# Kernel optimization log

Hardware: AMD Instinct MI355X
Metric: run time of the kernel (lower is better)

Reference implementation:

```python
import jax, jax.numpy as jnp
import numpy as np

LATENT = 1024
HID = 512
J = 24
# SMPL kinematic tree (parent[0] = -1 is the root, unused in the loop)
PARENT = [-1, 0, 0, 0, 1, 2, 3, 4, 5, 6, 7, 8, 9, 9, 9, 12, 13, 14, 16, 17, 18, 19, 20, 21]
EPS = 1e-12  # F.normalize default eps


def setup_inputs() -> dict:
    key = jax.random.key(0)
    k1, k2, k3, k4, k5 = jax.random.split(key, 5)
    B = 32768
    # Kaiming-uniform-ish init scales for the Linear layers
    s1 = 1.0 / np.sqrt(LATENT)
    s2 = 1.0 / np.sqrt(HID)
    return {
        "z": jax.random.normal(k1, (B, LATENT), dtype=jnp.float32),
        "W1": jax.random.uniform(k2, (LATENT, HID), minval=-s1, maxval=s1, dtype=jnp.float32),
        "b1": jax.random.uniform(k3, (HID,), minval=-s1, maxval=s1, dtype=jnp.float32),
        "W2": jax.random.uniform(k4, (HID, (J - 1) * 4), minval=-s2, maxval=s2, dtype=jnp.float32),
        "b2": jax.random.uniform(k5, ((J - 1) * 4,), minval=-s2, maxval=s2, dtype=jnp.float32),
    }


def reference(z, W1, b1, W2, b2):
    B = z.shape[0]
    h = jax.nn.silu(z @ W1 + b1)                    # [B, 512]
    raw = (h @ W2 + b2).reshape(B, J - 1, 4)        # [B, J-1, 4]
    vec = raw[..., :3]                              # [B, J-1, 3]
    norm = jnp.linalg.norm(vec, axis=-1, keepdims=True)
    direction = vec / jnp.maximum(norm, EPS)        # F.normalize(dim=-1)
    length = jax.nn.softplus(raw[..., 3])           # [B, J-1]
    child_off = direction * length[..., None]       # [B, J-1, 3]
    offsets = jnp.concatenate(
        [jnp.zeros((B, 1, 3), dtype=z.dtype), child_off], axis=1
    )                                                # [B, J, 3]
    # Static-tree forward kinematics: unroll the (small, fixed) joint loop.
    joints_list = [jnp.zeros((B, 3), dtype=z.dtype)]
    for j in range(1, J):
        joints_list.append(joints_list[PARENT[j]] + offsets[:, j])
    joints = jnp.stack(joints_list, axis=1)          # [B, J, 3]
    return (joints, offsets, length)
```

## Files before the change

### kernel.cpp

```cpp
#include <hip/hip_runtime.h>
#include <hip/hip_bf16.h>
#include <stdint.h>

#define BROWS 32768
#define LATENT 1024
#define HID 512

typedef float f32x4 __attribute__((ext_vector_type(4)));
typedef __bf16 bf16x8 __attribute__((ext_vector_type(8)));
typedef unsigned short us8 __attribute__((ext_vector_type(8)));

__device__ __forceinline__ void gload16(const void* g, void* l) {
  __builtin_amdgcn_global_load_lds(
      (__attribute__((address_space(1))) void*)g,
      (__attribute__((address_space(3))) void*)l, 16, 0, 0);
}

__device__ __forceinline__ void split_bf16(float x, unsigned short& hi, unsigned short& lo) {
  __bf16 h = (__bf16)x;
  float r = x - (float)h;
  __bf16 l = (__bf16)r;
  hi = __builtin_bit_cast(unsigned short, h);
  lo = __builtin_bit_cast(unsigned short, l);
}

__device__ __forceinline__ f32x4 mfma16(bf16x8 a, bf16x8 b, f32x4 c) {
  return __builtin_amdgcn_mfma_f32_16x16x32_bf16(a, b, c, 0, 0, 0);
}

__device__ __forceinline__ bf16x8 ldfrag(const unsigned short* p) {
  return __builtin_bit_cast(bf16x8, *(const us8*)p);
}

__global__ __launch_bounds__(256) void k_prep_w1t(const float* __restrict__ W1,
                                                  unsigned short* __restrict__ hi,
                                                  unsigned short* __restrict__ lo) {
  __shared__ float t[64][65];
  const int i = threadIdx.x;
  const int k0 = blockIdx.x * 64;
  const int n0 = blockIdx.y * 64;
#pragma unroll
  for (int s = 0; s < 4; s++) {
    const int r = s * 16 + (i >> 4);
    const int c = (i & 15) * 4;
    float4 v = *(const float4*)&W1[(size_t)(k0 + r) * HID + n0 + c];
    t[r][c] = v.x; t[r][c + 1] = v.y; t[r][c + 2] = v.z; t[r][c + 3] = v.w;
  }
  __syncthreads();
#pragma unroll
  for (int s = 0; s < 4; s++) {
    const int n = s * 16 + (i >> 4);
    const int k = (i & 15) * 4;
    unsigned short h[4], l[4];
#pragma unroll
    for (int j = 0; j < 4; j++) split_bf16(t[k + j][n], h[j], l[j]);
    *(ushort4*)&hi[(size_t)(n0 + n) * LATENT + k0 + k] = make_ushort4(h[0], h[1], h[2], h[3]);
    *(ushort4*)&lo[(size_t)(n0 + n) * LATENT + k0 + k] = make_ushort4(l[0], l[1], l[2], l[3]);
  }
}

__global__ __launch_bounds__(256) void k_prep_w2t(const float* __restrict__ W2,
                                                  unsigned short* __restrict__ hi,
                                                  unsigned short* __restrict__ lo) {
  const int idx = blockIdx.x * 256 + threadIdx.x;
  const int n = idx >> 9, k = idx & 511;
  const float v = (n < 92) ? W2[(size_t)k * 92 + n] : 0.0f;
  unsigned short h, l;
  split_bf16(v, h, l);
  hi[idx] = h;
  lo[idx] = l;
}

__global__ __launch_bounds__(256, 2) void k_gemm1(
    const float* __restrict__ z, const unsigned short* __restrict__ w1h,
    const unsigned short* __restrict__ w1l, const float* __restrict__ b1,
    unsigned short* __restrict__ hh, unsigned short* __restrict__ hl) {
  __shared__ unsigned short Ah[2][4096], Al[2][4096];
  __shared__ unsigned short Bh[2][4096], Bl[2][4096];

  const int tid = threadIdx.x;
  const int bid = blockIdx.x;
  const int swz = (bid & 7) * 128 + (bid >> 3);
  const int m0 = (swz >> 2) * 128;
  const int n0 = (swz & 3) * 128;

  const int w = tid >> 6, lane = tid & 63;
  const int wr = w >> 1, wc = w & 1;
  const int l15 = lane & 15, lg = lane >> 4;

  const int arow = tid >> 3;
  const int acol = (tid & 7) << 2;
  const int brow = tid >> 2;
  const int bc8 = (tid & 3) << 3;

  const float* zb = z + (size_t)(m0 + arow) * LATENT + acol;
  const unsigned short* w1hb = w1h + (size_t)(n0 + brow) * LATENT + bc8;
  const unsigned short* w1lb = w1l + (size_t)(n0 + brow) * LATENT + bc8;

  f32x4 acc[4][4] = {};
  float4 zr[4];

#define G1_STAGE_Z(kt) { \
    const float* p_ = zb + (kt) * 32; \
    zr[0] = *(const float4*)(p_); \
    zr[1] = *(const float4*)(p_ + 32 * LATENT); \
    zr[2] = *(const float4*)(p_ + 64 * LATENT); \
    zr[3] = *(const float4*)(p_ + 96 * LATENT); }

#define G1_STAGE_B(kt, bf) { \
    gload16(w1hb + (kt) * 32,               &Bh[bf][(w << 9)]); \
    gload16(w1hb + (kt) * 32 + 64 * LATENT, &Bh[bf][2048 + (w << 9)]); \
    gload16(w1lb + (kt) * 32,               &Bl[bf][(w << 9)]); \
    gload16(w1lb + (kt) * 32 + 64 * LATENT, &Bl[bf][2048 + (w << 9)]); }

#define G1_WRITE_A(bf) { \
    _Pragma("unroll") \
    for (int s_ = 0; s_ < 4; s_++) { \
      unsigned short h0, h1, h2, h3, l0, l1, l2, l3; \
      split_bf16(zr[s_].x, h0, l0); split_bf16(zr[s_].y, h1, l1); \
      split_bf16(zr[s_].z, h2, l2); split_bf16(zr[s_].w, h3, l3); \
      const int o_ = ((s_ * 32 + arow) << 5) + acol; \
      *(ushort4*)&Ah[bf][o_] = make_ushort4(h0, h1, h2, h3); \
      *(ushort4*)&Al[bf][o_] = make_ushort4(l0, l1, l2, l3); \
    } }

#define G1_COMPUTE(bf) { \
    bf16x8 ah[4], al[4], bh[4], bl[4]; \
    _Pragma("unroll") \
    for (int mf = 0; mf < 4; mf++) { \
      const int o_ = ((wr * 64 + mf * 16 + l15) << 5) + (lg << 3); \
      ah[mf] = ldfrag(&Ah[bf][o_]); \
      al[mf] = ldfrag(&Al[bf][o_]); \
    } \
    _Pragma("unroll") \
    for (int nf = 0; nf < 4; nf++) { \
      const int o_ = ((wc * 64 + nf * 16 + l15) << 5) + (lg << 3); \
      bh[nf] = ldfrag(&Bh[bf][o_]); \
      bl[nf] = ldfrag(&Bl[bf][o_]); \
    } \
    _Pragma("unroll") \
    for (int mf = 0; mf < 4; mf++) { \
      _Pragma("unroll") \
      for (int nf = 0; nf < 4; nf++) { \
        acc[mf][nf] = mfma16(ah[mf], bh[nf], acc[mf][nf]); \
        acc[mf][nf] = mfma16(al[mf], bh[nf], acc[mf][nf]); \
        acc[mf][nf] = mfma16(ah[mf], bl[nf], acc[mf][nf]); \
      } } }

  G1_STAGE_Z(0);
  G1_STAGE_B(0, 0);
  G1_WRITE_A(0);
  __syncthreads();

#pragma unroll 2
  for (int kt = 0; kt < 32; kt++) {
    const int cur = kt & 1, nx = cur ^ 1;
    if (kt < 31) {
      G1_STAGE_Z(kt + 1);
      G1_STAGE_B(kt + 1, nx);
    }
    G1_COMPUTE(cur);
    if (kt < 31) G1_WRITE_A(nx);
    __syncthreads();
  }

  float b1v[4];
#pragma unroll
  for (int nf = 0; nf < 4; nf++) b1v[nf] = b1[n0 + wc * 64 + nf * 16 + l15];

#pragma unroll
  for (int mf = 0; mf < 4; mf++) {
#pragma unroll
    for (int nf = 0; nf < 4; nf++) {
#pragma unroll
      for (int r = 0; r < 4; r++) {
        const int gm = m0 + wr * 64 + mf * 16 + (lg << 2) + r;
        const int gn = n0 + wc * 64 + nf * 16 + l15;
        const float x = acc[mf][nf][r] + b1v[nf];
        const float hval = x / (1.0f + expf(-x));
        unsigned short hi_, lo_;
        split_bf16(hval, hi_, lo_);
        const size_t o = (size_t)gm * HID + gn;
        hh[o] = hi_;
        hl[o] = lo_;
      }
    }
  }
}

__global__ __launch_bounds__(256, 2) void k_gemm2(
    const unsigned short* __restrict__ hh, const unsigned short* __restrict__ hl,
    const unsigned short* __restrict__ w2h, const unsigned short* __restrict__ w2l,
    const float* __restrict__ b2, float* __restrict__ out) {
  __shared__ unsigned short Ah[2][2048], Al[2][2048];
  __shared__ unsigned short Bh[2][4096], Bl[2][4096];
  __shared__ float raw[64][97];

  const int tid = threadIdx.x;
  const int m0 = blockIdx.x * 64;
  const int w = tid >> 6, lane = tid & 63;
  const int wr = w >> 1, wc = w & 1;
  const int l15 = lane & 15, lg = lane >> 4;
  const int arow = tid >> 2, ac8 = (tid & 3) << 3;

  const unsigned short* hhb = hh + (size_t)(m0 + arow) * HID + ac8;
  const unsigned short* hlb = hl + (size_t)(m0 + arow) * HID + ac8;
  const unsigned short* w2hb = w2h + (size_t)arow * HID + ac8;
  const unsigned short* w2lb = w2l + (size_t)arow * HID + ac8;

  f32x4 acc[2][3] = {};

#define G2_STAGE(kt, bf) { \
    gload16(hhb + (kt) * 32, &Ah[bf][(w << 9)]); \
    gload16(hlb + (kt) * 32, &Al[bf][(w << 9)]); \
    gload16(w2hb + (kt) * 32,            &Bh[bf][(w << 9)]); \
    gload16(w2hb + (kt) * 32 + 64 * HID, &Bh[bf][2048 + (w << 9)]); \
    gload16(w2lb + (kt) * 32,            &Bl[bf][(w << 9)]); \
    gload16(w2lb + (kt) * 32 + 64 * HID, &Bl[bf][2048 + (w << 9)]); }

#define G2_COMPUTE(bf) { \
    bf16x8 ah[2], al[2], bh[3], bl[3]; \
    _Pragma("unroll") \
    for (int mf = 0; mf < 2; mf++) { \
      const int o_ = ((wr * 32 + mf * 16 + l15) << 5) + (lg << 3); \
      ah[mf] = ldfrag(&Ah[bf][o_]); \
      al[mf] = ldfrag(&Al[bf][o_]); \
    } \
    _Pragma("unroll") \
    for (int nf = 0; nf < 3; nf++) { \
      const int o_ = ((wc * 48 + nf * 16 + l15) << 5) + (lg << 3); \
      bh[nf] = ldfrag(&Bh[bf][o_]); \
      bl[nf] = ldfrag(&Bl[bf][o_]); \
    } \
    _Pragma("unroll") \
    for (int mf = 0; mf < 2; mf++) { \
      _Pragma("unroll") \
      for (int nf = 0; nf < 3; nf++) { \
        acc[mf][nf] = mfma16(ah[mf], bh[nf], acc[mf][nf]); \
        acc[mf][nf] = mfma16(al[mf], bh[nf], acc[mf][nf]); \
        acc[mf][nf] = mfma16(ah[mf], bl[nf], acc[mf][nf]); \
      } } }

  G2_STAGE(0, 0);
  __syncthreads();
#pragma unroll 2
  for (int kt = 0; kt < 16; kt++) {
    const int cur = kt & 1, nx = cur ^ 1;
    if (kt < 15) G2_STAGE(kt + 1, nx);
    G2_COMPUTE(cur);
    __syncthreads();
  }

#pragma unroll
  for (int mf = 0; mf < 2; mf++) {
#pragma unroll
    for (int nf = 0; nf < 3; nf++) {
#pragma unroll
      for (int r = 0; r < 4; r++) {
        const int ml = wr * 32 + mf * 16 + (lg << 2) + r;
        const int nl = wc * 48 + nf * 16 + l15;
        raw[ml][nl] = acc[mf][nf][r];
      }
    }
  }
  __syncthreads();

  const size_t OFFB = (size_t)BROWS * 72;
  const size_t LENB = (size_t)BROWS * 144;

  for (int task = tid; task < 64 * 24; task += 256) {
    const int row = task / 24;
    const int j = task - row * 24;
    const int gm = m0 + row;
    float* orow = out + OFFB + (size_t)gm * 72;
    if (j == 0) {
      orow[0] = 0.0f; orow[1] = 0.0f; orow[2] = 0.0f;
    } else {
      const int c0 = (j - 1) * 4;
      const float vx = raw[row][c0 + 0] + b2[c0 + 0];
      const float vy = raw[row][c0 + 1] + b2[c0 + 1];
      const float vz = raw[row][c0 + 2] + b2[c0 + 2];
      const float wv = raw[row][c0 + 3] + b2[c0 + 3];
      const float nrm = sqrtf(vx * vx + vy * vy + vz * vz);
      const float inv = 1.0f / fmaxf(nrm, 1e-12f);
      const float len = fmaxf(wv, 0.0f) + log1pf(expf(-fabsf(wv)));
      const float sc = inv * len;
      const float ox = vx * sc, oy = vy * sc, oz = vz * sc;
      orow[j * 3 + 0] = ox; orow[j * 3 + 1] = oy; orow[j * 3 + 2] = oz;
      out[LENB + (size_t)gm * 23 + (j - 1)] = len;
      raw[row][c0 + 0] = ox; raw[row][c0 + 1] = oy; raw[row][c0 + 2] = oz;
    }
  }
  __syncthreads();

  if (tid < 64) {
    constexpr int PAR[24] = {-1, 0, 0, 0, 1, 2, 3, 4, 5, 6, 7, 8,
                             9, 9, 9, 12, 13, 14, 16, 17, 18, 19, 20, 21};
    const int gm = m0 + tid;
    float e[72];
    e[0] = 0.0f; e[1] = 0.0f; e[2] = 0.0f;
#pragma unroll
    for (int j = 1; j < 24; j++) {
      const int p = PAR[j];
      const int c0 = (j - 1) * 4;
      e[3 * j + 0] = e[3 * p + 0] + raw[tid][c0 + 0];
      e[3 * j + 1] = e[3 * p + 1] + raw[tid][c0 + 1];
      e[3 * j + 2] = e[3 * p + 2] + raw[tid][c0 + 2];
    }
    float4* jo = (float4*)(out + (size_t)gm * 72);
#pragma unroll
    for (int q = 0; q < 18; q++)
      jo[q] = make_float4(e[4 * q + 0], e[4 * q + 1], e[4 * q + 2], e[4 * q + 3]);
  }
}

extern "C" void kernel_launch(void* const* d_in, const int* in_sizes, int n_in,
                              void* d_out, int out_size, void* d_ws, size_t ws_size,
                              hipStream_t stream) {
  const float* z = (const float*)d_in[0];
  const float* W1 = (const float*)d_in[1];
  const float* b1 = (const float*)d_in[2];
  const float* W2 = (const float*)d_in[3];
  const float* b2 = (const float*)d_in[4];
  float* out = (float*)d_out;

  char* ws = (char*)d_ws;
  unsigned short* w1h = (unsigned short*)(ws);
  unsigned short* w1l = (unsigned short*)(ws + (1 << 20));
  unsigned short* w2h = (unsigned short*)(ws + (2 << 20));
  unsigned short* w2l = (unsigned short*)(ws + (2 << 20) + 131072);
  unsigned short* hh = (unsigned short*)(ws + ((size_t)4 << 20));
  unsigned short* hl = (unsigned short*)(ws + ((size_t)4 << 20) + ((size_t)32 << 20));

  hipLaunchKernelGGL(k_prep_w1t, dim3(16, 8), dim3(256), 0, stream, W1, w1h, w1l);
  hipLaunchKernelGGL(k_prep_w2t, dim3(256), dim3(256), 0, stream, W2, w2h, w2l);
  hipLaunchKernelGGL(k_gemm1, dim3(1024), dim3(256), 0, stream, z, w1h, w1l, b1, hh, hl);
  hipLaunchKernelGGL(k_gemm2, dim3(512), dim3(256), 0, stream, hh, hl, w2h, w2l, b2, out);
}
```

Measured before the change: 164.6 us.

## Restructure gemm1 pipeline with swizzled LDS, 8x2 wave tiling and fine-grained waitcnt scheduling

Rewrites the first GEMM kernel's main loop. All operands now live in one byte-addressed LDS buffer with XOR-swizzled layouts to avoid bank conflicts. Each wave covers 128 rows by 32 columns instead of a 2x2 wave grid of 64x64 tiles. Each K step is split into three MFMA phases (hi*hi, lo*hi, hi*lo), with global loads for the next tile interleaved between them and explicit vmcnt/lgkmcnt waits, sched_barriers and s_setprio. The block swizzle changes so blocks sharing an N tile run together. The aim is better overlap of global memory traffic with MFMA work and fewer LDS conflicts, at the risk of fragile manual wait counts and more A-fragment register pressure.

Measured after the change: 166.7 us. About the same (+1.3%).

```diff
diff --git a/kernel.cpp b/kernel.cpp
--- a/kernel.cpp
+++ b/kernel.cpp
@@ -28,7 +28,7 @@
   return __builtin_amdgcn_mfma_f32_16x16x32_bf16(a, b, c, 0, 0, 0);
 }
 
-__device__ __forceinline__ bf16x8 ldfrag(const unsigned short* p) {
+__device__ __forceinline__ bf16x8 ldfrag(const void* p) {
   return __builtin_bit_cast(bf16x8, *(const us8*)p);
 }
 
@@ -75,107 +75,153 @@
     const float* __restrict__ z, const unsigned short* __restrict__ w1h,
     const unsigned short* __restrict__ w1l, const float* __restrict__ b1,
     unsigned short* __restrict__ hh, unsigned short* __restrict__ hl) {
-  __shared__ unsigned short Ah[2][4096], Al[2][4096];
-  __shared__ unsigned short Bh[2][4096], Bl[2][4096];
+  __shared__ __attribute__((aligned(16))) unsigned short lds_u[32768];
+  char* lb = (char*)lds_u;
 
   const int tid = threadIdx.x;
   const int bid = blockIdx.x;
   const int swz = (bid & 7) * 128 + (bid >> 3);
-  const int m0 = (swz >> 2) * 128;
-  const int n0 = (swz & 3) * 128;
-
-  const int w = tid >> 6, lane = tid & 63;
-  const int wr = w >> 1, wc = w & 1;
-  const int l15 = lane & 15, lg = lane >> 4;
-
-  const int arow = tid >> 3;
-  const int acol = (tid & 7) << 2;
-  const int brow = tid >> 2;
-  const int bc8 = (tid & 3) << 3;
-
-  const float* zb = z + (size_t)(m0 + arow) * LATENT + acol;
-  const unsigned short* w1hb = w1h + (size_t)(n0 + brow) * LATENT + bc8;
-  const unsigned short* w1lb = w1l + (size_t)(n0 + brow) * LATENT + bc8;
-
-  f32x4 acc[4][4] = {};
+  const int nb = swz >> 8;
+  const int mb = swz & 255;
+  const int m0 = mb * 128;
+  const int n0g = nb * 128;
+
+  const int wv = tid >> 6, l = tid & 63;
+  const int l15 = l & 15, lg = l >> 4;
+
+  const int abase = l15 * 64 + ((lg ^ ((l15 >> 1) & 3)) << 4);
+
+  const float* zbase = z + (size_t)(m0 + (tid >> 3)) * LATENT + (tid & 7) * 4;
+  const int wbyte = (tid >> 3) * 64 + (((tid & 7) * 8) ^ (((tid >> 4) & 3) << 4));
+
+  const size_t bsrc = (size_t)(n0g + 32 * wv + (l >> 2)) * LATENT +
+                      ((((l & 3) ^ ((l >> 3) & 3))) << 3);
+
+  f32x4 acc[8][2] = {};
   float4 zr[4];
-
-#define G1_STAGE_Z(kt) { \
-    const float* p_ = zb + (kt) * 32; \
-    zr[0] = *(const float4*)(p_); \
-    zr[1] = *(const float4*)(p_ + 32 * LATENT); \
-    zr[2] = *(const float4*)(p_ + 64 * LATENT); \
-    zr[3] = *(const float4*)(p_ + 96 * LATENT); }
-
-#define G1_STAGE_B(kt, bf) { \
-    gload16(w1hb + (kt) * 32,               &Bh[bf][(w << 9)]); \
-    gload16(w1hb + (kt) * 32 + 64 * LATENT, &Bh[bf][2048 + (w << 9)]); \
-    gload16(w1lb + (kt) * 32,               &Bl[bf][(w << 9)]); \
-    gload16(w1lb + (kt) * 32 + 64 * LATENT, &Bl[bf][2048 + (w << 9)]); }
-
-#define G1_WRITE_A(bf) { \
-    _Pragma("unroll") \
-    for (int s_ = 0; s_ < 4; s_++) { \
-      unsigned short h0, h1, h2, h3, l0, l1, l2, l3; \
-      split_bf16(zr[s_].x, h0, l0); split_bf16(zr[s_].y, h1, l1); \
-      split_bf16(zr[s_].z, h2, l2); split_bf16(zr[s_].w, h3, l3); \
-      const int o_ = ((s_ * 32 + arow) << 5) + acol; \
-      *(ushort4*)&Ah[bf][o_] = make_ushort4(h0, h1, h2, h3); \
-      *(ushort4*)&Al[bf][o_] = make_ushort4(l0, l1, l2, l3); \
-    } }
-
-#define G1_COMPUTE(bf) { \
-    bf16x8 ah[4], al[4], bh[4], bl[4]; \
-    _Pragma("unroll") \
-    for (int mf = 0; mf < 4; mf++) { \
-      const int o_ = ((wr * 64 + mf * 16 + l15) << 5) + (lg << 3); \
-      ah[mf] = ldfrag(&Ah[bf][o_]); \
-      al[mf] = ldfrag(&Al[bf][o_]); \
-    } \
-    _Pragma("unroll") \
-    for (int nf = 0; nf < 4; nf++) { \
-      const int o_ = ((wc * 64 + nf * 16 + l15) << 5) + (lg << 3); \
-      bh[nf] = ldfrag(&Bh[bf][o_]); \
-      bl[nf] = ldfrag(&Bl[bf][o_]); \
-    } \
-    _Pragma("unroll") \
-    for (int mf = 0; mf < 4; mf++) { \
-      _Pragma("unroll") \
-      for (int nf = 0; nf < 4; nf++) { \
-        acc[mf][nf] = mfma16(ah[mf], bh[nf], acc[mf][nf]); \
-        acc[mf][nf] = mfma16(al[mf], bh[nf], acc[mf][nf]); \
-        acc[mf][nf] = mfma16(ah[mf], bl[nf], acc[mf][nf]); \
-      } } }
-
-  G1_STAGE_Z(0);
-  G1_STAGE_B(0, 0);
-  G1_WRITE_A(0);
-  __syncthreads();
+  bf16x8 ah[8], bhf[2], blf[2];
+
+#define AHO 0
+#define ALO 8192
+#define BHO 16384
+#define BLO 24576
+
+#define ISSUE_A(kt1)                                                         \
+  {                                                                          \
+    _Pragma("unroll") for (int i_ = 0; i_ < 4; i_++)                         \
+        zr[i_] = *(const float4*)(zbase + (size_t)(32 * i_) * LATENT + (kt1) * 32); \
+  }
+
+#define ISSUE_B(arr, kt1, dstoff, j_)                                        \
+  gload16(arr + bsrc + (size_t)(16 * (j_)) * LATENT + (kt1) * 32,            \
+          lb + (dstoff) + (wv * 2 + (j_)) * 1024);
+
+#define WRITE_A(dstAh, dstAl)                                                \
+  {                                                                          \
+    _Pragma("unroll") for (int i_ = 0; i_ < 4; i_++) {                       \
+      unsigned short h0, h1, h2, h3, q0, q1, q2, q3;                         \
+      split_bf16(zr[i_].x, h0, q0); split_bf16(zr[i_].y, h1, q1);            \
+      split_bf16(zr[i_].z, h2, q2); split_bf16(zr[i_].w, h3, q3);            \
+      *(ushort4*)(lb + (dstAh) + wbyte + i_ * 2048) = make_ushort4(h0, h1, h2, h3); \
+      *(ushort4*)(lb + (dstAl) + wbyte + i_ * 2048) = make_ushort4(q0, q1, q2, q3); \
+    }                                                                        \
+  }
+
+#define LD_AFRAGS(dst, roff)                                                 \
+  {                                                                          \
+    _Pragma("unroll") for (int mf = 0; mf < 8; mf++)                         \
+        dst[mf] = ldfrag(lb + (roff) + abase + mf * 1024);                   \
+  }
+
+#define LD_BFRAGS(dst, roff)                                                 \
+  {                                                                          \
+    _Pragma("unroll") for (int nf = 0; nf < 2; nf++)                         \
+        dst[nf] = ldfrag(lb + (roff) + wv * 2048 + nf * 1024 + abase);       \
+  }
+
+#define DO_MFMA(AF, BF)                                                      \
+  {                                                                          \
+    __builtin_amdgcn_s_setprio(1);                                           \
+    _Pragma("unroll") for (int mf = 0; mf < 8; mf++)                         \
+        _Pragma("unroll") for (int nf = 0; nf < 2; nf++)                     \
+            acc[mf][nf] = mfma16(AF[mf], BF[nf], acc[mf][nf]);               \
+    __builtin_amdgcn_s_setprio(0);                                           \
+  }
+
+#define SBAR  __builtin_amdgcn_s_barrier()
+#define SCH0  __builtin_amdgcn_sched_barrier(0)
+
+  ISSUE_A(0);
+  SCH0;
+  ISSUE_B(w1h, 0, BHO, 0); ISSUE_B(w1h, 0, BHO, 1);
+  ISSUE_B(w1l, 0, BLO, 0); ISSUE_B(w1l, 0, BLO, 1);
+  SCH0;
+  asm volatile("s_waitcnt vmcnt(4)" ::: "memory");
+  SCH0;
+  WRITE_A(AHO, ALO);
+  asm volatile("s_waitcnt lgkmcnt(0)" ::: "memory");
+  SBAR; SCH0;
 
 #pragma unroll 2
-  for (int kt = 0; kt < 32; kt++) {
-    const int cur = kt & 1, nx = cur ^ 1;
-    if (kt < 31) {
-      G1_STAGE_Z(kt + 1);
-      G1_STAGE_B(kt + 1, nx);
-    }
-    G1_COMPUTE(cur);
-    if (kt < 31) G1_WRITE_A(nx);
-    __syncthreads();
-  }
-
-  float b1v[4];
-#pragma unroll
-  for (int nf = 0; nf < 4; nf++) b1v[nf] = b1[n0 + wc * 64 + nf * 16 + l15];
-
-#pragma unroll
-  for (int mf = 0; mf < 4; mf++) {
-#pragma unroll
-    for (int nf = 0; nf < 4; nf++) {
+  for (int t = 0; t < 32; ++t) {
+    const int cur = (t & 1) * 32768;
+    const int nxt = cur ^ 32768;
+    const bool last = (t == 31);
+
+    asm volatile("s_waitcnt vmcnt(1)" ::: "memory");
+    SCH0;
+    LD_AFRAGS(ah, cur + AHO);
+    LD_BFRAGS(bhf, cur + BHO);
+    if (!last) {
+      ISSUE_A(t + 1);
+      SCH0;
+      ISSUE_B(w1h, t + 1, nxt + BHO, 0);
+    }
+    SBAR; SCH0;
+    DO_MFMA(ah, bhf);
+    SBAR; SCH0;
+
+    {
+      bf16x8 alf[8];
+      LD_AFRAGS(alf, cur + ALO);
+      if (!last) {
+        ISSUE_B(w1h, t + 1, nxt + BHO, 1);
+        ISSUE_B(w1l, t + 1, nxt + BLO, 0);
+      }
+      SBAR; SCH0;
+      DO_MFMA(alf, bhf);
+      SBAR; SCH0;
+    }
+
+    if (!last) { asm volatile("s_waitcnt vmcnt(7)" ::: "memory"); }
+    else       { asm volatile("s_waitcnt vmcnt(0)" ::: "memory"); }
+    SCH0;
+    LD_BFRAGS(blf, cur + BLO);
+    if (!last) {
+      ISSUE_B(w1l, t + 1, nxt + BLO, 1);
+      asm volatile("s_waitcnt vmcnt(3)" ::: "memory");
+      SCH0;
+      WRITE_A(nxt + AHO, nxt + ALO);
+      asm volatile("s_waitcnt lgkmcnt(0)" ::: "memory");
+      SCH0;
+    }
+    SBAR; SCH0;
+    DO_MFMA(ah, blf);
+    SBAR; SCH0;
+  }
+
+  float b1v[2];
+#pragma unroll
+  for (int nf = 0; nf < 2; nf++) b1v[nf] = b1[n0g + wv * 32 + nf * 16 + l15];
+
+#pragma unroll
+  for (int mf = 0; mf < 8; mf++)
+#pragma unroll
+    for (int nf = 0; nf < 2; nf++)
 #pragma unroll
       for (int r = 0; r < 4; r++) {
-        const int gm = m0 + wr * 64 + mf * 16 + (lg << 2) + r;
-        const int gn = n0 + wc * 64 + nf * 16 + l15;
+        const int gm = m0 + mf * 16 + (lg << 2) + r;
+        const int gn = n0g + wv * 32 + nf * 16 + l15;
         const float x = acc[mf][nf][r] + b1v[nf];
         const float hval = x / (1.0f + expf(-x));
         unsigned short hi_, lo_;
@@ -184,8 +230,11 @@
         hh[o] = hi_;
         hl[o] = lo_;
       }
-    }
-  }
+
+#undef AHO
+#undef ALO
+#undef BHO
+#undef BLO
 }
 
 __global__ __launch_bounds__(256, 2) void k_gemm2(
```

## Restructure gemm1 into 256x256 tiles with swizzled fused hi/lo LDS layout

Applied to the files above, without the earlier changes.

The GEMM1 tile grows from 128x128 with 4 waves to 256x256 with 8 waves in 128KB of dynamic LDS. W1 is pre-packed into a fused, XOR-swizzled hi/lo bf16 layout so that B loads go straight to LDS and fragment reads avoid bank conflicts. The main loop is rescheduled with explicit waitcnt, raw barriers, setprio around the MFMA clusters, and prefetch of z two steps ahead, to raise data reuse and overlap loads with compute. In exchange, register pressure rises (32 accumulators per wave), and with only 256 blocks occupancy is low, which risks tail imbalance across the 256 CUs.

Result: faster. 151.1 us (-8.2%).

```diff
diff --git a/kernel.cpp b/kernel.cpp
--- a/kernel.cpp
+++ b/kernel.cpp
@@ -28,35 +28,28 @@
   return __builtin_amdgcn_mfma_f32_16x16x32_bf16(a, b, c, 0, 0, 0);
 }
 
-__device__ __forceinline__ bf16x8 ldfrag(const unsigned short* p) {
+__device__ __forceinline__ bf16x8 ldfrag(const void* p) {
   return __builtin_bit_cast(bf16x8, *(const us8*)p);
 }
 
-__global__ __launch_bounds__(256) void k_prep_w1t(const float* __restrict__ W1,
-                                                  unsigned short* __restrict__ hi,
-                                                  unsigned short* __restrict__ lo) {
-  __shared__ float t[64][65];
-  const int i = threadIdx.x;
-  const int k0 = blockIdx.x * 64;
-  const int n0 = blockIdx.y * 64;
-#pragma unroll
-  for (int s = 0; s < 4; s++) {
-    const int r = s * 16 + (i >> 4);
-    const int c = (i & 15) * 4;
-    float4 v = *(const float4*)&W1[(size_t)(k0 + r) * HID + n0 + c];
-    t[r][c] = v.x; t[r][c + 1] = v.y; t[r][c + 2] = v.z; t[r][c + 3] = v.w;
-  }
-  __syncthreads();
-#pragma unroll
-  for (int s = 0; s < 4; s++) {
-    const int n = s * 16 + (i >> 4);
-    const int k = (i & 15) * 4;
-    unsigned short h[4], l[4];
-#pragma unroll
-    for (int j = 0; j < 4; j++) split_bf16(t[k + j][n], h[j], l[j]);
-    *(ushort4*)&hi[(size_t)(n0 + n) * LATENT + k0 + k] = make_ushort4(h[0], h[1], h[2], h[3]);
-    *(ushort4*)&lo[(size_t)(n0 + n) * LATENT + k0 + k] = make_ushort4(l[0], l[1], l[2], l[3]);
-  }
+__global__ __launch_bounds__(256) void k_prep_w1f(const float* __restrict__ W1,
+                                                  unsigned short* __restrict__ w1f) {
+  const int n = blockIdx.x;
+  const int t = threadIdx.x;
+  const int kt = t >> 3, ls = t & 7;
+  const int p = ls ^ (n & 7);
+  const int k0 = kt * 32 + (ls & 3) * 8;
+  unsigned short v[8];
+#pragma unroll
+  for (int e = 0; e < 8; e++) {
+    const float x = W1[(size_t)(k0 + e) * HID + n];
+    unsigned short h, q;
+    split_bf16(x, h, q);
+    v[e] = (ls < 4) ? h : q;
+  }
+  unsigned short* dst = w1f + ((size_t)n * 32 + kt) * 64 + p * 8;
+  *(ushort4*)(dst) = make_ushort4(v[0], v[1], v[2], v[3]);
+  *(ushort4*)(dst + 4) = make_ushort4(v[4], v[5], v[6], v[7]);
 }
 
 __global__ __launch_bounds__(256) void k_prep_w2t(const float* __restrict__ W2,
@@ -71,111 +64,137 @@
   lo[idx] = l;
 }
 
-__global__ __launch_bounds__(256, 2) void k_gemm1(
-    const float* __restrict__ z, const unsigned short* __restrict__ w1h,
-    const unsigned short* __restrict__ w1l, const float* __restrict__ b1,
+__global__ __launch_bounds__(512, 2) void k_gemm1(
+    const float* __restrict__ z, const unsigned short* __restrict__ w1f,
+    const float* __restrict__ b1,
     unsigned short* __restrict__ hh, unsigned short* __restrict__ hl) {
-  __shared__ unsigned short Ah[2][4096], Al[2][4096];
-  __shared__ unsigned short Bh[2][4096], Bl[2][4096];
+  extern __shared__ __align__(16) char lb[];
 
   const int tid = threadIdx.x;
   const int bid = blockIdx.x;
-  const int swz = (bid & 7) * 128 + (bid >> 3);
-  const int m0 = (swz >> 2) * 128;
-  const int n0 = (swz & 3) * 128;
-
-  const int w = tid >> 6, lane = tid & 63;
-  const int wr = w >> 1, wc = w & 1;
-  const int l15 = lane & 15, lg = lane >> 4;
+  const int swzb = (bid & 7) * 32 + (bid >> 3);
+  const int mb = swzb >> 1, nbk = swzb & 1;
+  const int m0 = mb * 256, n0g = nbk * 256;
+
+  const int wv = tid >> 6, l = tid & 63;
+  const int wr = wv >> 2, wc = wv & 3;
+  const int l15 = l & 15, lg = l >> 4;
+  const int xr = l15 & 7;
+
+  const int ahB = (wr * 128 + l15) * 128 + ((lg ^ xr) << 4);
+  const int alB = (wr * 128 + l15) * 128 + ((((4 | lg) ^ xr)) << 4);
+  const int bhB = 32768 + (wc * 64 + l15) * 128 + ((lg ^ xr) << 4);
+  const int blB = 32768 + (wc * 64 + l15) * 128 + ((((4 | lg) ^ xr)) << 4);
 
   const int arow = tid >> 3;
-  const int acol = (tid & 7) << 2;
-  const int brow = tid >> 2;
-  const int bc8 = (tid & 3) << 3;
-
-  const float* zb = z + (size_t)(m0 + arow) * LATENT + acol;
-  const unsigned short* w1hb = w1h + (size_t)(n0 + brow) * LATENT + bc8;
-  const unsigned short* w1lb = w1l + (size_t)(n0 + brow) * LATENT + bc8;
-
-  f32x4 acc[4][4] = {};
+  const int kc4 = tid & 7;
+  const int xw = arow & 7;
+  const int hi_off = (((kc4 >> 1) ^ xw) << 4) + (kc4 & 1) * 8;
+  const int lo_off = ((((4 | (kc4 >> 1)) ^ xw)) << 4) + (kc4 & 1) * 8;
+  const float* zb = z + (size_t)(m0 + arow) * LATENT + kc4 * 4;
+
+  const unsigned short* bsrc =
+      w1f + ((size_t)(n0g + wv * 32 + (l >> 3)) * 32) * 64 + (l & 7) * 8;
+
+  f32x4 acc[8][4] = {};
   float4 zr[4];
 
-#define G1_STAGE_Z(kt) { \
-    const float* p_ = zb + (kt) * 32; \
-    zr[0] = *(const float4*)(p_); \
-    zr[1] = *(const float4*)(p_ + 32 * LATENT); \
-    zr[2] = *(const float4*)(p_ + 64 * LATENT); \
-    zr[3] = *(const float4*)(p_ + 96 * LATENT); }
-
-#define G1_STAGE_B(kt, bf) { \
-    gload16(w1hb + (kt) * 32,               &Bh[bf][(w << 9)]); \
-    gload16(w1hb + (kt) * 32 + 64 * LATENT, &Bh[bf][2048 + (w << 9)]); \
-    gload16(w1lb + (kt) * 32,               &Bl[bf][(w << 9)]); \
-    gload16(w1lb + (kt) * 32 + 64 * LATENT, &Bl[bf][2048 + (w << 9)]); }
-
-#define G1_WRITE_A(bf) { \
-    _Pragma("unroll") \
-    for (int s_ = 0; s_ < 4; s_++) { \
-      unsigned short h0, h1, h2, h3, l0, l1, l2, l3; \
-      split_bf16(zr[s_].x, h0, l0); split_bf16(zr[s_].y, h1, l1); \
-      split_bf16(zr[s_].z, h2, l2); split_bf16(zr[s_].w, h3, l3); \
-      const int o_ = ((s_ * 32 + arow) << 5) + acol; \
-      *(ushort4*)&Ah[bf][o_] = make_ushort4(h0, h1, h2, h3); \
-      *(ushort4*)&Al[bf][o_] = make_ushort4(l0, l1, l2, l3); \
-    } }
-
-#define G1_COMPUTE(bf) { \
-    bf16x8 ah[4], al[4], bh[4], bl[4]; \
-    _Pragma("unroll") \
-    for (int mf = 0; mf < 4; mf++) { \
-      const int o_ = ((wr * 64 + mf * 16 + l15) << 5) + (lg << 3); \
-      ah[mf] = ldfrag(&Ah[bf][o_]); \
-      al[mf] = ldfrag(&Al[bf][o_]); \
-    } \
-    _Pragma("unroll") \
-    for (int nf = 0; nf < 4; nf++) { \
-      const int o_ = ((wc * 64 + nf * 16 + l15) << 5) + (lg << 3); \
-      bh[nf] = ldfrag(&Bh[bf][o_]); \
-      bl[nf] = ldfrag(&Bl[bf][o_]); \
-    } \
-    _Pragma("unroll") \
-    for (int mf = 0; mf < 4; mf++) { \
-      _Pragma("unroll") \
-      for (int nf = 0; nf < 4; nf++) { \
-        acc[mf][nf] = mfma16(ah[mf], bh[nf], acc[mf][nf]); \
-        acc[mf][nf] = mfma16(al[mf], bh[nf], acc[mf][nf]); \
-        acc[mf][nf] = mfma16(ah[mf], bl[nf], acc[mf][nf]); \
-      } } }
-
-  G1_STAGE_Z(0);
-  G1_STAGE_B(0, 0);
-  G1_WRITE_A(0);
-  __syncthreads();
+#define LOAD_ZR(kt1)                                                          \
+  {                                                                           \
+    _Pragma("unroll") for (int i_ = 0; i_ < 4; i_++)                          \
+        zr[i_] = *(const float4*)(zb + (size_t)(64 * i_) * LATENT + (kt1) * 32); \
+  }
+
+#define WRITE_A(bufo)                                                         \
+  {                                                                           \
+    _Pragma("unroll") for (int i_ = 0; i_ < 4; i_++) {                        \
+      unsigned short h0, h1, h2, h3, q0, q1, q2, q3;                          \
+      split_bf16(zr[i_].x, h0, q0); split_bf16(zr[i_].y, h1, q1);             \
+      split_bf16(zr[i_].z, h2, q2); split_bf16(zr[i_].w, h3, q3);             \
+      char* rp = lb + (bufo) + (arow + 64 * i_) * 128;                        \
+      *(ushort4*)(rp + hi_off) = make_ushort4(h0, h1, h2, h3);                \
+      *(ushort4*)(rp + lo_off) = make_ushort4(q0, q1, q2, q3);                \
+    }                                                                         \
+  }
+
+#define GLOAD_B(bufo, kt1)                                                    \
+  {                                                                           \
+    _Pragma("unroll") for (int j_ = 0; j_ < 4; j_++)                          \
+        gload16(bsrc + (size_t)j_ * 16384 + (kt1) * 64,                       \
+                lb + (bufo) + 32768 + (wv * 32 + j_ * 8) * 128);              \
+  }
+
+#define MCLUSTER(AF, BF)                                                      \
+  {                                                                           \
+    __builtin_amdgcn_s_setprio(1);                                            \
+    _Pragma("unroll") for (int mf = 0; mf < 8; mf++)                          \
+        _Pragma("unroll") for (int nf = 0; nf < 4; nf++)                      \
+            acc[mf][nf] = mfma16(AF[mf], BF[nf], acc[mf][nf]);                \
+    __builtin_amdgcn_s_setprio(0);                                            \
+  }
+
+  GLOAD_B(0, 0);
+  LOAD_ZR(0);
+  asm volatile("s_waitcnt vmcnt(0)" ::: "memory");
+  WRITE_A(0);
+  LOAD_ZR(1);
+  asm volatile("s_waitcnt lgkmcnt(0)" ::: "memory");
+  __builtin_amdgcn_s_barrier();
+  __builtin_amdgcn_sched_barrier(0);
 
 #pragma unroll 2
-  for (int kt = 0; kt < 32; kt++) {
-    const int cur = kt & 1, nx = cur ^ 1;
-    if (kt < 31) {
-      G1_STAGE_Z(kt + 1);
-      G1_STAGE_B(kt + 1, nx);
-    }
-    G1_COMPUTE(cur);
-    if (kt < 31) G1_WRITE_A(nx);
-    __syncthreads();
+  for (int t = 0; t < 32; ++t) {
+    const int cb = (t & 1) * 65536;
+    const int nb2 = cb ^ 65536;
+
+    bf16x8 ah[8], bh[4];
+#pragma unroll
+    for (int mf = 0; mf < 8; mf++) ah[mf] = ldfrag(lb + cb + ahB + mf * 2048);
+#pragma unroll
+    for (int nf = 0; nf < 4; nf++) bh[nf] = ldfrag(lb + cb + bhB + nf * 2048);
+
+    if (t < 31) {
+      WRITE_A(nb2);
+      GLOAD_B(nb2, t + 1);
+      asm volatile("" ::: "memory");
+      if (t < 30) LOAD_ZR(t + 2);
+    }
+
+    MCLUSTER(ah, bh);
+
+    {
+      bf16x8 alf[8];
+#pragma unroll
+      for (int mf = 0; mf < 8; mf++) alf[mf] = ldfrag(lb + cb + alB + mf * 2048);
+      MCLUSTER(alf, bh);
+    }
+
+    {
+      bf16x8 blf[4];
+#pragma unroll
+      for (int nf = 0; nf < 4; nf++) blf[nf] = ldfrag(lb + cb + blB + nf * 2048);
+      MCLUSTER(ah, blf);
+    }
+
+    if (t < 30) { asm volatile("s_waitcnt vmcnt(4)" ::: "memory"); }
+    else        { asm volatile("s_waitcnt vmcnt(0)" ::: "memory"); }
+    asm volatile("s_waitcnt lgkmcnt(0)" ::: "memory");
+    __builtin_amdgcn_s_barrier();
+    __builtin_amdgcn_sched_barrier(0);
   }
 
   float b1v[4];
 #pragma unroll
-  for (int nf = 0; nf < 4; nf++) b1v[nf] = b1[n0 + wc * 64 + nf * 16 + l15];
-
-#pragma unroll
-  for (int mf = 0; mf < 4; mf++) {
-#pragma unroll
-    for (int nf = 0; nf < 4; nf++) {
+  for (int nf = 0; nf < 4; nf++) b1v[nf] = b1[n0g + wc * 64 + nf * 16 + l15];
+
+#pragma unroll
+  for (int mf = 0; mf < 8; mf++)
+#pragma unroll
+    for (int nf = 0; nf < 4; nf++)
 #pragma unroll
       for (int r = 0; r < 4; r++) {
-        const int gm = m0 + wr * 64 + mf * 16 + (lg << 2) + r;
-        const int gn = n0 + wc * 64 + nf * 16 + l15;
+        const int gm = m0 + wr * 128 + mf * 16 + (lg << 2) + r;
+        const int gn = n0g + wc * 64 + nf * 16 + l15;
         const float x = acc[mf][nf][r] + b1v[nf];
         const float hval = x / (1.0f + expf(-x));
         unsigned short hi_, lo_;
@@ -184,8 +203,6 @@
         hh[o] = hi_;
         hl[o] = lo_;
       }
-    }
-  }
 }
 
 __global__ __launch_bounds__(256, 2) void k_gemm2(
@@ -219,26 +236,26 @@
     gload16(w2lb + (kt) * 32 + 64 * HID, &Bl[bf][2048 + (w << 9)]); }
 
 #define G2_COMPUTE(bf) { \
-    bf16x8 ah[2], al[2], bh[3], bl[3]; \
+    bf16x8 ah2[2], al2[2], bh2[3], bl2[3]; \
     _Pragma("unroll") \
     for (int mf = 0; mf < 2; mf++) { \
       const int o_ = ((wr * 32 + mf * 16 + l15) << 5) + (lg << 3); \
-      ah[mf] = ldfrag(&Ah[bf][o_]); \
-      al[mf] = ldfrag(&Al[bf][o_]); \
+      ah2[mf] = ldfrag(&Ah[bf][o_]); \
+      al2[mf] = ldfrag(&Al[bf][o_]); \
     } \
     _Pragma("unroll") \
     for (int nf = 0; nf < 3; nf++) { \
       const int o_ = ((wc * 48 + nf * 16 + l15) << 5) + (lg << 3); \
-      bh[nf] = ldfrag(&Bh[bf][o_]); \
-      bl[nf] = ldfrag(&Bl[bf][o_]); \
+      bh2[nf] = ldfrag(&Bh[bf][o_]); \
+      bl2[nf] = ldfrag(&Bl[bf][o_]); \
     } \
     _Pragma("unroll") \
     for (int mf = 0; mf < 2; mf++) { \
       _Pragma("unroll") \
       for (int nf = 0; nf < 3; nf++) { \
-        acc[mf][nf] = mfma16(ah[mf], bh[nf], acc[mf][nf]); \
-        acc[mf][nf] = mfma16(al[mf], bh[nf], acc[mf][nf]); \
-        acc[mf][nf] = mfma16(ah[mf], bl[nf], acc[mf][nf]); \
+        acc[mf][nf] = mfma16(ah2[mf], bh2[nf], acc[mf][nf]); \
+        acc[mf][nf] = mfma16(al2[mf], bh2[nf], acc[mf][nf]); \
+        acc[mf][nf] = mfma16(ah2[mf], bl2[nf], acc[mf][nf]); \
       } } }
 
   G2_STAGE(0, 0);
@@ -280,10 +297,10 @@
       const float vx = raw[row][c0 + 0] + b2[c0 + 0];
       const float vy = raw[row][c0 + 1] + b2[c0 + 1];
       const float vz = raw[row][c0 + 2] + b2[c0 + 2];
-      const float wv = raw[row][c0 + 3] + b2[c0 + 3];
+      const float wvv = raw[row][c0 + 3] + b2[c0 + 3];
       const float nrm = sqrtf(vx * vx + vy * vy + vz * vz);
       const float inv = 1.0f / fmaxf(nrm, 1e-12f);
-      const float len = fmaxf(wv, 0.0f) + log1pf(expf(-fabsf(wv)));
+      const float len = fmaxf(wvv, 0.0f) + log1pf(expf(-fabsf(wvv)));
       const float sc = inv * len;
       const float ox = vx * sc, oy = vy * sc, oz = vz * sc;
       orow[j * 3 + 0] = ox; orow[j * 3 + 1] = oy; orow[j * 3 + 2] = oz;
@@ -325,15 +342,19 @@
   float* out = (float*)d_out;
 
   char* ws = (char*)d_ws;
-  unsigned short* w1h = (unsigned short*)(ws);
-  unsigned short* w1l = (unsigned short*)(ws + (1 << 20));
+  unsigned short* w1f = (unsigned short*)(ws);
   unsigned short* w2h = (unsigned short*)(ws + (2 << 20));
   unsigned short* w2l = (unsigned short*)(ws + (2 << 20) + 131072);
   unsigned short* hh = (unsigned short*)(ws + ((size_t)4 << 20));
   unsigned short* hl = (unsigned short*)(ws + ((size_t)4 << 20) + ((size_t)32 << 20));
 
-  hipLaunchKernelGGL(k_prep_w1t, dim3(16, 8), dim3(256), 0, stream, W1, w1h, w1l);
+  static bool attr_set = false;
+  (void)attr_set;
+  hipFuncSetAttribute((const void*)k_gemm1,
+                      hipFuncAttributeMaxDynamicSharedMemorySize, 131072);
+
+  hipLaunchKernelGGL(k_prep_w1f, dim3(512), dim3(256), 0, stream, W1, w1f);
   hipLaunchKernelGGL(k_prep_w2t, dim3(256), dim3(256), 0, stream, W2, w2h, w2l);
-  hipLaunchKernelGGL(k_gemm1, dim3(1024), dim3(256), 0, stream, z, w1h, w1l, b1, hh, hl);
+  hipLaunchKernelGGL(k_gemm1, dim3(256), dim3(512), 131072, stream, z, w1f, b1, hh, hl);
   hipLaunchKernelGGL(k_gemm2, dim3(512), dim3(256), 0, stream, hh, hl, w2h, w2l, b2, out);
 }
```
